# Kernel tuning notes

Measured on AMD Instinct MI355X. Metric: run time of the kernel, lower is better.

Reference implementation:

```python
import jax, jax.numpy as jnp
import numpy as np

IN_FEATURES = 1024
N_CLASSES = 50257
CUTOFFS = [2000, 10000]      # head covers [0,2000); clusters [2000,10000), [10000,50257)
DIV_VALUE = 4.0
IGNORE_INDEX = -1
N_ROWS = 4096
HEAD_SIZE = CUTOFFS[0] + len(CUTOFFS)  # 2002 (head classes + one slot per tail cluster)
HSZ = [int(IN_FEATURES // (DIV_VALUE ** (i + 1))) for i in range(len(CUTOFFS))]  # [256, 64]
BOUNDS = CUTOFFS + [N_CLASSES]


def setup_inputs() -> dict:
    key = jax.random.key(0)
    ks = jax.random.split(key, 8)
    x = jax.random.normal(ks[0], (N_ROWS, IN_FEATURES), dtype=jnp.float32)
    target = jax.random.randint(ks[1], (N_ROWS,), 0, N_CLASSES, dtype=jnp.int64)
    drop = jax.random.uniform(ks[2], (N_ROWS,)) < 0.1
    target = jnp.where(drop, IGNORE_INDEX, target)
    s = 1.0 / np.sqrt(IN_FEATURES)
    head_w = jax.random.normal(ks[3], (HEAD_SIZE, IN_FEATURES), dtype=jnp.float32) * s
    proj0 = jax.random.normal(ks[4], (HSZ[0], IN_FEATURES), dtype=jnp.float32) * s
    out0 = jax.random.normal(ks[5], (BOUNDS[1] - BOUNDS[0], HSZ[0]), dtype=jnp.float32) * (1.0 / np.sqrt(HSZ[0]))
    proj1 = jax.random.normal(ks[6], (HSZ[1], IN_FEATURES), dtype=jnp.float32) * s
    out1 = jax.random.normal(ks[7], (BOUNDS[2] - BOUNDS[1], HSZ[1]), dtype=jnp.float32) * (1.0 / np.sqrt(HSZ[1]))
    return {"x": x, "target": target, "head_w": head_w,
            "proj0": proj0, "out0": out0, "proj1": proj1, "out1": out1}


def reference(x, target, head_w, proj0, out0, proj1, out1):
    # head: [N, cutoff0 + n_clusters] logits, shared log-softmax
    head_lp = jax.nn.log_softmax(jnp.einsum('nd,hd->nh', x, head_w), axis=-1)
    rows = jnp.arange(x.shape[0])
    valid = target != IGNORE_INDEX
    t = jnp.where(valid, target, 0)

    # head-band targets: log prob directly from head
    t_head = jnp.clip(t, 0, CUTOFFS[0] - 1)
    logp = head_lp[rows, t_head]

    # tail clusters: head cluster-slot logprob + within-cluster logprob
    tails = [(proj0, out0), (proj1, out1)]
    for i, (proj, out) in enumerate(tails):
        low, high = BOUNDS[i], BOUNDS[i + 1]
        # [N, hsz] @ [hsz, osz] -> [N, osz] cluster logits
        cl_lp = jax.nn.log_softmax(
            jnp.einsum('nh,oh->no', jnp.einsum('nd,hd->nh', x, proj), out), axis=-1)
        rel = jnp.clip(t - low, 0, high - low - 1)
        cand = head_lp[:, CUTOFFS[0] + i] + cl_lp[rows, rel]
        logp = jnp.where((t >= low) & (t < high), cand, logp)

    # ignore-index filter + mean == masked mean over valid rows
    vf = valid.astype(logp.dtype)
    loss = -(logp * vf).sum() / vf.sum()
    return loss
```

## Files before the change

kernel.cpp:

```cpp
#include <hip/hip_runtime.h>
#include <hip/hip_bf16.h>

typedef __attribute__((ext_vector_type(8))) short bf16x8;
typedef __attribute__((ext_vector_type(4))) float f32x4;
typedef unsigned short u16;

constexpr int NR      = 4096;
constexpr int INF     = 1024;
constexpr int HEAD_N  = 2002;
constexpr int HEAD_NP = 2048;
constexpr int C0_LO   = 2000, C0_HI = 10000;
constexpr int C0_N    = 8000;
constexpr int C0_NP   = 8064;
constexpr int C1_N    = 40257;
constexpr int C1_NP   = 40320;
constexpr int K0      = 256;
constexpr int K1      = 64;
constexpr int PCAT    = 320;
constexpr int PCAT_P  = 384;
constexpr int WCAT_R  = HEAD_NP + PCAT_P;
constexpr int IGNORE  = -1;
constexpr float LOG2E = 1.4426950408889634f;
constexpr float LN2   = 0.6931471805599453f;

static __device__ __forceinline__ u16 f32_to_bf16(float f) {
    unsigned int u = __float_as_uint(f);
    return (u16)((u + 0x7FFFu + ((u >> 16) & 1u)) >> 16);
}

static __device__ __forceinline__ float fast_exp2(float x) {
#if __has_builtin(__builtin_amdgcn_exp2f)
    return __builtin_amdgcn_exp2f(x);
#else
    return __expf(x * LN2);
#endif
}

static __device__ __forceinline__ void gload_lds16(const u16* g, u16* l) {
    __builtin_amdgcn_global_load_lds(
        (const __attribute__((address_space(1))) unsigned int*)g,
        (__attribute__((address_space(3))) unsigned int*)l, 16, 0, 0);
}

struct CvtSegs { const float* s[6]; u16* d[6]; int n8[6]; float sc[6]; };

__global__ void cvt_multi(CvtSegs segs) {
    const int stride = gridDim.x * blockDim.x;
    const int gid = blockIdx.x * blockDim.x + threadIdx.x;
#pragma unroll
    for (int seg = 0; seg < 6; ++seg) {
        const float4* sp = (const float4*)segs.s[seg];
        bf16x8* dp = (bf16x8*)segs.d[seg];
        const int n8 = segs.n8[seg];
        const float sc = segs.sc[seg];
        for (int i = gid; i < n8; i += stride) {
            float4 a = sp[2 * i], b = sp[2 * i + 1];
            bf16x8 o;
            o[0] = (short)f32_to_bf16(a.x * sc); o[1] = (short)f32_to_bf16(a.y * sc);
            o[2] = (short)f32_to_bf16(a.z * sc); o[3] = (short)f32_to_bf16(a.w * sc);
            o[4] = (short)f32_to_bf16(b.x * sc); o[5] = (short)f32_to_bf16(b.y * sc);
            o[6] = (short)f32_to_bf16(b.z * sc); o[7] = (short)f32_to_bf16(b.w * sc);
            dp[i] = o;
        }
    }
}

__launch_bounds__(256, 2)
__global__ void fused_headproj(const u16* __restrict__ A, const u16* __restrict__ B,
                               const int* __restrict__ tgt,
                               float* __restrict__ SEH, float* __restrict__ TL,
                               float* __restrict__ HF, u16* __restrict__ HB)
{
    constexpr int K = INF;
    __shared__ u16 ldsA[128 * 64];
    __shared__ u16 ldsB[128 * 64];
    __shared__ int sth[128];
    const int tid  = threadIdx.x;
    const int wid  = tid >> 6;
    const int lane = tid & 63;
    const int wr   = wid >> 1;
    const int wc   = wid & 1;
    const int row0 = blockIdx.x * 128;
    const int col0 = blockIdx.y * 128;
    const bool expmode = (blockIdx.y < HEAD_NP / 128);

    if (expmode && tid < 128) {
        int t = tgt[row0 + tid];
        sth[tid] = (t < 0) ? 0 : (t < C0_LO ? t : (t < C0_HI ? C0_LO : C0_LO + 1));
    }

    f32x4 acc[4][4];
#pragma unroll
    for (int m = 0; m < 4; ++m)
#pragma unroll
        for (int n = 0; n < 4; ++n) acc[m][n] = (f32x4){0.f, 0.f, 0.f, 0.f};

    const int srow = lane >> 3;
    const int ssw  = (lane & 7) ^ srow;

    for (int ks = 0; ks < K / 64; ++ks) {
        const int k0 = ks * 64;
#pragma unroll
        for (int q = 0; q < 4; ++q) {
            const int c   = q * 4 + wid;
            const int row = c * 8 + srow;
            gload_lds16(A + (size_t)(row0 + row) * K + k0 + ssw * 8, ldsA + c * 512);
        }
#pragma unroll
        for (int q = 0; q < 4; ++q) {
            const int c   = q * 4 + wid;
            const int row = c * 8 + srow;
            gload_lds16(B + (size_t)(col0 + row) * K + k0 + ssw * 8, ldsB + c * 512);
        }
        __syncthreads();

        const bf16x8* A8 = (const bf16x8*)ldsA;
        const bf16x8* B8 = (const bf16x8*)ldsB;
        bf16x8 af[4][2], bf[4][2];
#pragma unroll
        for (int m = 0; m < 4; ++m) {
            const int ar = wr * 64 + m * 16 + (lane & 15);
#pragma unroll
            for (int ksub = 0; ksub < 2; ++ksub) {
                const int slot = ksub * 4 + (lane >> 4);
                af[m][ksub] = A8[ar * 8 + (slot ^ (ar & 7))];
            }
        }
#pragma unroll
        for (int n = 0; n < 4; ++n) {
            const int br = wc * 64 + n * 16 + (lane & 15);
#pragma unroll
            for (int ksub = 0; ksub < 2; ++ksub) {
                const int slot = ksub * 4 + (lane >> 4);
                bf[n][ksub] = B8[br * 8 + (slot ^ (br & 7))];
            }
        }
#pragma unroll
        for (int ksub = 0; ksub < 2; ++ksub)
#pragma unroll
            for (int m = 0; m < 4; ++m)
#pragma unroll
                for (int n = 0; n < 4; ++n)
                    acc[m][n] = __builtin_amdgcn_mfma_f32_16x16x32_bf16(
                        af[m][ksub], bf[n][ksub], acc[m][n], 0, 0, 0);
        __syncthreads();
    }

    if (expmode) {
#pragma unroll
        for (int m = 0; m < 4; ++m) {
            f32x4 rs = (f32x4){0.f, 0.f, 0.f, 0.f};
#pragma unroll
            for (int n = 0; n < 4; ++n) {
                const int cls = col0 + wc * 64 + n * 16 + (lane & 15);
                if (cls < HEAD_N) {
#pragma unroll
                    for (int r = 0; r < 4; ++r) {
                        rs[r] += fast_exp2(acc[m][n][r]);
                        const int lrow = wr * 64 + m * 16 + (lane >> 4) * 4 + r;
                        if (sth[lrow] == cls) TL[row0 + lrow] = acc[m][n][r];
                    }
                }
            }
#pragma unroll
            for (int msk = 1; msk < 16; msk <<= 1) {
#pragma unroll
                for (int r = 0; r < 4; ++r) rs[r] += __shfl_xor(rs[r], msk, 64);
            }
            if ((lane & 15) == 0) {
                const int rb = row0 + wr * 64 + m * 16 + (lane >> 4) * 4;
#pragma unroll
                for (int r = 0; r < 4; ++r) atomicAdd(&SEH[rb + r], rs[r]);
            }
        }
    } else {
        const int pc0 = col0 - HEAD_NP;
#pragma unroll
        for (int m = 0; m < 4; ++m) {
#pragma unroll
            for (int n = 0; n < 4; ++n) {
                const int col = pc0 + wc * 64 + n * 16 + (lane & 15);
                if (col < PCAT) {
#pragma unroll
                    for (int r = 0; r < 4; ++r) {
                        const int row = row0 + wr * 64 + m * 16 + (lane >> 4) * 4 + r;
                        const float v = acc[m][n][r];
                        HF[(size_t)row * PCAT + col] = v;
                        HB[(size_t)row * PCAT + col] = f32_to_bf16(v);
                    }
                }
            }
        }
    }
}

template<int K, int CT>
__launch_bounds__(256, 2)
__global__ void sumexp_stream(const u16* __restrict__ H, int ldh,
                              const u16* __restrict__ W,
                              int nreal, int tps, int ntiles,
                              float* __restrict__ SE)
{
    constexpr int MSETS = 2;
    constexpr int NKF   = K / 32;
    constexpr int SLOTS = K / 8;
    constexpr int NT    = CT / 16;
    constexpr int CHUNKS = CT * K * 2 / 4096;
    constexpr int RPC   = 256 / SLOTS;
    __shared__ u16 ldsB[2][CT * K];

    const int tid  = threadIdx.x;
    const int wid  = tid >> 6;
    const int lane = tid & 63;
    const int row0 = blockIdx.x * (4 * MSETS * 16) + wid * (MSETS * 16);

    const int t0 = blockIdx.y * tps;
    const int t1 = min(t0 + tps, ntiles);
    if (t0 >= t1) return;

    bf16x8 afr[MSETS][NKF];
#pragma unroll
    for (int m = 0; m < MSETS; ++m) {
        const u16* hr = H + (size_t)(row0 + m * 16 + (lane & 15)) * ldh + (lane >> 4) * 8;
#pragma unroll
        for (int kf = 0; kf < NKF; ++kf)
            afr[m][kf] = *(const bf16x8*)(hr + kf * 32);
    }

    float rs[MSETS][4];
#pragma unroll
    for (int m = 0; m < MSETS; ++m)
#pragma unroll
        for (int r = 0; r < 4; ++r) rs[m][r] = 0.f;

    const int trow   = tid / SLOTS;
    const int swoff  = ((tid % SLOTS) ^ (trow & 7)) * 8;

    auto STAGE = [&](int t, int buf) {
        const u16* wb = W + (size_t)t * CT * K + (size_t)trow * K + swoff;
        u16* lb = &ldsB[buf][wid * 512];
#pragma unroll
        for (int c = 0; c < CHUNKS; ++c)
            gload_lds16(wb + (size_t)c * RPC * K, lb + c * 2048);
    };

    int cur = 0;
    STAGE(t0, 0);
    __syncthreads();

    for (int t = t0; t < t1; ++t) {
        if (t + 1 < t1) STAGE(t + 1, cur ^ 1);

        const bf16x8* B8 = (const bf16x8*)ldsB[cur];
        const bool full = (t + 1) * CT <= nreal;
#pragma unroll
        for (int n = 0; n < NT; ++n) {
            const int br = n * 16 + (lane & 15);
            bf16x8 bfr[NKF];
#pragma unroll
            for (int kf = 0; kf < NKF; ++kf)
                bfr[kf] = B8[br * SLOTS + ((kf * 4 + (lane >> 4)) ^ (br & 7))];
            f32x4 acc[MSETS];
#pragma unroll
            for (int m = 0; m < MSETS; ++m) acc[m] = (f32x4){0.f, 0.f, 0.f, 0.f};
#pragma unroll
            for (int m = 0; m < MSETS; ++m)
#pragma unroll
                for (int kf = 0; kf < NKF; ++kf)
                    acc[m] = __builtin_amdgcn_mfma_f32_16x16x32_bf16(
                        afr[m][kf], bfr[kf], acc[m], 0, 0, 0);
            if (full) {
#pragma unroll
                for (int m = 0; m < MSETS; ++m)
#pragma unroll
                    for (int r = 0; r < 4; ++r) rs[m][r] += fast_exp2(acc[m][r]);
            } else {
                const int cls = t * CT + n * 16 + (lane & 15);
                if (cls < nreal) {
#pragma unroll
                    for (int m = 0; m < MSETS; ++m)
#pragma unroll
                        for (int r = 0; r < 4; ++r) rs[m][r] += fast_exp2(acc[m][r]);
                }
            }
        }
        __syncthreads();
        cur ^= 1;
    }

#pragma unroll
    for (int msk = 1; msk < 16; msk <<= 1)
#pragma unroll
        for (int m = 0; m < MSETS; ++m)
#pragma unroll
            for (int r = 0; r < 4; ++r)
                rs[m][r] += __shfl_xor(rs[m][r], msk, 64);
    if ((lane & 15) == 0) {
        const int rb = row0 + (lane >> 4) * 4;
#pragma unroll
        for (int m = 0; m < MSETS; ++m)
#pragma unroll
            for (int r = 0; r < 4; ++r)
                atomicAdd(&SE[rb + m * 16 + r], rs[m][r]);
    }
}

__global__ void epilogue_kernel(const int* __restrict__ tgt, const float* __restrict__ tl,
                                const float* __restrict__ out0, const float* __restrict__ out1,
                                const float* __restrict__ hcatf,
                                const float* __restrict__ se_head, const float* __restrict__ se_c0,
                                const float* __restrict__ se_c1,
                                float* __restrict__ rowlogp, float* __restrict__ rowvalid) {
    const int wid = threadIdx.x >> 6, lane = threadIdx.x & 63;
    const int r = blockIdx.x * 4 + wid;
    const int t = tgt[r];
    const bool valid = (t != IGNORE);
    const int tc = valid ? t : 0;
    const int band = (tc < C0_LO) ? 0 : (tc < C0_HI) ? 1 : 2;

    float p2 = 0.f;
    if (band == 1) {
        const float* hr = hcatf + (size_t)r * PCAT;
        const float* cr = out0 + (size_t)(tc - C0_LO) * K0;
        for (int k = lane; k < K0; k += 64) p2 += hr[k] * cr[k];
    } else if (band == 2) {
        p2 = hcatf[(size_t)r * PCAT + 256 + lane] * out1[(size_t)(tc - C0_HI) * K1 + lane];
    }
#pragma unroll
    for (int msk = 32; msk >= 1; msk >>= 1) p2 += __shfl_xor(p2, msk, 64);

    if (lane == 0) {
        float logp = LN2 * tl[r] - __logf(se_head[r]);
        if (band == 1)      logp += p2 - __logf(se_c0[r]);
        else if (band == 2) logp += p2 - __logf(se_c1[r]);
        rowlogp[r]  = valid ? logp : 0.f;
        rowvalid[r] = valid ? 1.f : 0.f;
    }
}

__global__ void final_reduce(const float* __restrict__ rowlogp,
                             const float* __restrict__ rowvalid, float* __restrict__ out) {
    __shared__ float sl[256], sv[256];
    const int tid = threadIdx.x;
    float a = 0.f, b = 0.f;
    for (int i = tid; i < NR; i += 256) { a += rowlogp[i]; b += rowvalid[i]; }
    sl[tid] = a; sv[tid] = b;
    __syncthreads();
    for (int s = 128; s > 0; s >>= 1) {
        if (tid < s) { sl[tid] += sl[tid + s]; sv[tid] += sv[tid + s]; }
        __syncthreads();
    }
    if (tid == 0) out[0] = -sl[0] / sv[0];
}

extern "C" void kernel_launch(void* const* d_in, const int* in_sizes, int n_in,
                              void* d_out, int out_size, void* d_ws, size_t ws_size,
                              hipStream_t stream) {
    const float* x      = (const float*)d_in[0];
    const int*   tgt    = (const int*)d_in[1];
    const float* head_w = (const float*)d_in[2];
    const float* proj0  = (const float*)d_in[3];
    const float* out0   = (const float*)d_in[4];
    const float* proj1  = (const float*)d_in[5];
    const float* out1   = (const float*)d_in[6];
    float* loss = (float*)d_out;

    char* base = (char*)d_ws;
    size_t off = 0;
    auto alloc = [&](size_t bytes) { char* p = base + off; off += (bytes + 255) & ~(size_t)255; return p; };

    u16* xb    = (u16*)alloc((size_t)NR * INF * 2);
    u16* wcatb = (u16*)alloc((size_t)WCAT_R * INF * 2);
    u16* o0b   = (u16*)alloc((size_t)C0_NP * K0 * 2);
    u16* o1b   = (u16*)alloc((size_t)C1_NP * K1 * 2);
    float* hcatf = (float*)alloc((size_t)NR * PCAT * 4);
    u16*   hcatb = (u16*)alloc((size_t)NR * PCAT * 2);
    float* se_head = (float*)alloc((size_t)NR * 4);
    float* se_c0   = (float*)alloc((size_t)NR * 4);
    float* se_c1   = (float*)alloc((size_t)NR * 4);
    float* tl       = (float*)alloc((size_t)NR * 4);
    float* rowlogp  = (float*)alloc((size_t)NR * 4);
    float* rowvalid = (float*)alloc((size_t)NR * 4);

    hipMemsetAsync(se_head, 0, (size_t)NR * 4, stream);
    hipMemsetAsync(se_c0,   0, (size_t)NR * 4, stream);
    hipMemsetAsync(se_c1,   0, (size_t)NR * 4, stream);

    CvtSegs segs;
    segs.s[0] = x;      segs.d[0] = xb;                              segs.n8[0] = NR * INF / 8;      segs.sc[0] = 1.0f;
    segs.s[1] = head_w; segs.d[1] = wcatb;                           segs.n8[1] = HEAD_N * INF / 8;  segs.sc[1] = LOG2E;
    segs.s[2] = proj0;  segs.d[2] = wcatb + (size_t)HEAD_NP * INF;   segs.n8[2] = 256 * INF / 8;     segs.sc[2] = 1.0f;
    segs.s[3] = proj1;  segs.d[3] = wcatb + (size_t)(HEAD_NP + 256) * INF; segs.n8[3] = 64 * INF / 8; segs.sc[3] = 1.0f;
    segs.s[4] = out0;   segs.d[4] = o0b;                             segs.n8[4] = C0_N * K0 / 8;     segs.sc[4] = LOG2E;
    segs.s[5] = out1;   segs.d[5] = o1b;                             segs.n8[5] = C1_N * K1 / 8;     segs.sc[5] = LOG2E;
    cvt_multi<<<2048, 256, 0, stream>>>(segs);

    fused_headproj<<<dim3(32, WCAT_R / 128), 256, 0, stream>>>(
        xb, wcatb, tgt, se_head, tl, hcatf, hcatb);

    sumexp_stream<K0, 32><<<dim3(32, 32), 256, 0, stream>>>(
        hcatb, PCAT, o0b, C0_N, 8, 250, se_c0);
    sumexp_stream<K1, 128><<<dim3(32, 40), 256, 0, stream>>>(
        hcatb + 256, PCAT, o1b, C1_N, 8, 315, se_c1);

    epilogue_kernel<<<NR / 4, 256, 0, stream>>>(tgt, tl, out0, out1, hcatf,
                                                se_head, se_c0, se_c1, rowlogp, rowvalid);
    final_reduce<<<1, 256, 0, stream>>>(rowlogp, rowvalid, loss);
    (void)in_sizes; (void)n_in; (void)out_size; (void)ws_size;
}
```

Baseline: 109.8 us.

## Compact tail-cluster rows by target and fuse head and cluster sumexp into one kernel

A new compaction kernel builds per-cluster row lists from the targets, so the cluster sum-exp GEMMs run only over rows whose target falls in that cluster instead of all 4096 rows. The head GEMM and both cluster sum-exp streams are merged into one interleaved mega-kernel launch, and the projection GEMM is split into its own small kernel. Atomics and memsets are replaced by per-split partial buffers that the epilogue reduces. This skips most of the cluster work, which is legitimate because the loss only needs the target row's cluster normaliser, at the cost of gather loads and an extra serial launch.

```diff
diff --git a/kernel.cpp b/kernel.cpp
--- a/kernel.cpp
+++ b/kernel.cpp
@@ -11,7 +11,6 @@
 constexpr int HEAD_NP = 2048;
 constexpr int C0_LO   = 2000, C0_HI = 10000;
 constexpr int C0_N    = 8000;
-constexpr int C0_NP   = 8064;
 constexpr int C1_N    = 40257;
 constexpr int C1_NP   = 40320;
 constexpr int K0      = 256;
@@ -22,6 +21,11 @@
 constexpr int IGNORE  = -1;
 constexpr float LOG2E = 1.4426950408889634f;
 constexpr float LN2   = 0.6931471805599453f;
+
+constexpr int S0      = 16;
+constexpr int S1      = 10;
+constexpr int NHP     = 32;
+constexpr int MEGA_GRID = 1024 + 512;
 
 static __device__ __forceinline__ u16 f32_to_bf16(float f) {
     unsigned int u = __float_as_uint(f);
@@ -65,26 +69,117 @@
     }
 }
 
+__global__ void compact_kernel(const int* __restrict__ tgt,
+                               int* __restrict__ c0list, int* __restrict__ c1list,
+                               int* __restrict__ crow, int* __restrict__ cnts) {
+    __shared__ int b0, b1;
+    if (threadIdx.x == 0) { b0 = 0; b1 = 0; }
+    __syncthreads();
+#pragma unroll
+    for (int i = 0; i < 4; ++i) {
+        const int r = threadIdx.x + i * 1024;
+        const int t = tgt[r];
+        if (t >= C0_LO && t < C0_HI) { int s = atomicAdd(&b0, 1); c0list[s] = r; crow[r] = s; }
+        else if (t >= C0_HI)         { int s = atomicAdd(&b1, 1); c1list[s] = r; crow[r] = s; }
+        else crow[r] = 0;
+    }
+    __syncthreads();
+    const int c0 = b0, c1 = b1;
+    const int p0 = (c0 + 127) & ~127, p1 = (c1 + 127) & ~127;
+    if (threadIdx.x == 0) { cnts[0] = c0; cnts[1] = c1; cnts[2] = p0; cnts[3] = p1; }
+    for (int i = c0 + (int)threadIdx.x; i < p0; i += 1024) c0list[i] = 0;
+    for (int i = c1 + (int)threadIdx.x; i < p1; i += 1024) c1list[i] = 0;
+}
+
 __launch_bounds__(256, 2)
-__global__ void fused_headproj(const u16* __restrict__ A, const u16* __restrict__ B,
-                               const int* __restrict__ tgt,
-                               float* __restrict__ SEH, float* __restrict__ TL,
-                               float* __restrict__ HF, u16* __restrict__ HB)
+__global__ void proj_tile(const u16* __restrict__ A, const u16* __restrict__ B,
+                          float* __restrict__ HF, u16* __restrict__ HB)
 {
     constexpr int K = INF;
     __shared__ u16 ldsA[128 * 64];
     __shared__ u16 ldsB[128 * 64];
-    __shared__ int sth[128];
-    const int tid  = threadIdx.x;
-    const int wid  = tid >> 6;
-    const int lane = tid & 63;
-    const int wr   = wid >> 1;
-    const int wc   = wid & 1;
-    const int row0 = blockIdx.x * 128;
-    const int col0 = blockIdx.y * 128;
-    const bool expmode = (blockIdx.y < HEAD_NP / 128);
-
-    if (expmode && tid < 128) {
+    const int tid = threadIdx.x, wid = tid >> 6, lane = tid & 63;
+    const int wr = wid >> 1, wc = wid & 1;
+    const int row0 = blockIdx.x * 128, col0 = blockIdx.y * 128;
+
+    f32x4 acc[4][4];
+#pragma unroll
+    for (int m = 0; m < 4; ++m)
+#pragma unroll
+        for (int n = 0; n < 4; ++n) acc[m][n] = (f32x4){0.f, 0.f, 0.f, 0.f};
+
+    const int srow = lane >> 3;
+    const int ssw  = (lane & 7) ^ srow;
+
+    for (int ks = 0; ks < K / 64; ++ks) {
+        const int k0 = ks * 64;
+#pragma unroll
+        for (int q = 0; q < 4; ++q) {
+            const int c = q * 4 + wid, row = c * 8 + srow;
+            gload_lds16(A + (size_t)(row0 + row) * K + k0 + ssw * 8, ldsA + c * 512);
+        }
+#pragma unroll
+        for (int q = 0; q < 4; ++q) {
+            const int c = q * 4 + wid, row = c * 8 + srow;
+            gload_lds16(B + (size_t)(col0 + row) * K + k0 + ssw * 8, ldsB + c * 512);
+        }
+        __syncthreads();
+        const bf16x8* A8 = (const bf16x8*)ldsA;
+        const bf16x8* B8 = (const bf16x8*)ldsB;
+        bf16x8 af[4][2], bfr[4][2];
+#pragma unroll
+        for (int m = 0; m < 4; ++m) {
+            const int ar = wr * 64 + m * 16 + (lane & 15);
+#pragma unroll
+            for (int ks2 = 0; ks2 < 2; ++ks2)
+                af[m][ks2] = A8[ar * 8 + ((ks2 * 4 + (lane >> 4)) ^ (ar & 7))];
+        }
+#pragma unroll
+        for (int n = 0; n < 4; ++n) {
+            const int br = wc * 64 + n * 16 + (lane & 15);
+#pragma unroll
+            for (int ks2 = 0; ks2 < 2; ++ks2)
+                bfr[n][ks2] = B8[br * 8 + ((ks2 * 4 + (lane >> 4)) ^ (br & 7))];
+        }
+#pragma unroll
+        for (int ks2 = 0; ks2 < 2; ++ks2)
+#pragma unroll
+            for (int m = 0; m < 4; ++m)
+#pragma unroll
+                for (int n = 0; n < 4; ++n)
+                    acc[m][n] = __builtin_amdgcn_mfma_f32_16x16x32_bf16(
+                        af[m][ks2], bfr[n][ks2], acc[m][n], 0, 0, 0);
+        __syncthreads();
+    }
+#pragma unroll
+    for (int m = 0; m < 4; ++m)
+#pragma unroll
+        for (int n = 0; n < 4; ++n) {
+            const int col = col0 + wc * 64 + n * 16 + (lane & 15);
+            if (col < PCAT) {
+#pragma unroll
+                for (int r = 0; r < 4; ++r) {
+                    const int row = row0 + wr * 64 + m * 16 + (lane >> 4) * 4 + r;
+                    const float v = acc[m][n][r];
+                    HF[(size_t)row * PCAT + col] = v;
+                    HB[(size_t)row * PCAT + col] = f32_to_bf16(v);
+                }
+            }
+        }
+}
+
+static __device__ void head_section(int rb, int ct,
+                                    const u16* __restrict__ A, const u16* __restrict__ B,
+                                    const int* __restrict__ tgt,
+                                    float* __restrict__ SEHp, float* __restrict__ TL,
+                                    u16* ldsA, u16* ldsB, int* sth)
+{
+    constexpr int K = INF;
+    const int tid = threadIdx.x, wid = tid >> 6, lane = tid & 63;
+    const int wr = wid >> 1, wc = wid & 1;
+    const int row0 = rb * 128, col0 = ct * 128;
+
+    if (tid < 128) {
         int t = tgt[row0 + tid];
         sth[tid] = (t < 0) ? 0 : (t < C0_LO ? t : (t < C0_HI ? C0_LO : C0_LO + 1));
     }
@@ -102,126 +197,97 @@
         const int k0 = ks * 64;
 #pragma unroll
         for (int q = 0; q < 4; ++q) {
-            const int c   = q * 4 + wid;
-            const int row = c * 8 + srow;
+            const int c = q * 4 + wid, row = c * 8 + srow;
             gload_lds16(A + (size_t)(row0 + row) * K + k0 + ssw * 8, ldsA + c * 512);
         }
 #pragma unroll
         for (int q = 0; q < 4; ++q) {
-            const int c   = q * 4 + wid;
-            const int row = c * 8 + srow;
+            const int c = q * 4 + wid, row = c * 8 + srow;
             gload_lds16(B + (size_t)(col0 + row) * K + k0 + ssw * 8, ldsB + c * 512);
         }
         __syncthreads();
-
         const bf16x8* A8 = (const bf16x8*)ldsA;
         const bf16x8* B8 = (const bf16x8*)ldsB;
-        bf16x8 af[4][2], bf[4][2];
+        bf16x8 af[4][2], bfr[4][2];
 #pragma unroll
         for (int m = 0; m < 4; ++m) {
             const int ar = wr * 64 + m * 16 + (lane & 15);
 #pragma unroll
-            for (int ksub = 0; ksub < 2; ++ksub) {
-                const int slot = ksub * 4 + (lane >> 4);
-                af[m][ksub] = A8[ar * 8 + (slot ^ (ar & 7))];
-            }
+            for (int ks2 = 0; ks2 < 2; ++ks2)
+                af[m][ks2] = A8[ar * 8 + ((ks2 * 4 + (lane >> 4)) ^ (ar & 7))];
         }
 #pragma unroll
         for (int n = 0; n < 4; ++n) {
             const int br = wc * 64 + n * 16 + (lane & 15);
 #pragma unroll
-            for (int ksub = 0; ksub < 2; ++ksub) {
-                const int slot = ksub * 4 + (lane >> 4);
-                bf[n][ksub] = B8[br * 8 + (slot ^ (br & 7))];
-            }
-        }
-#pragma unroll
-        for (int ksub = 0; ksub < 2; ++ksub)
+            for (int ks2 = 0; ks2 < 2; ++ks2)
+                bfr[n][ks2] = B8[br * 8 + ((ks2 * 4 + (lane >> 4)) ^ (br & 7))];
+        }
+#pragma unroll
+        for (int ks2 = 0; ks2 < 2; ++ks2)
 #pragma unroll
             for (int m = 0; m < 4; ++m)
 #pragma unroll
                 for (int n = 0; n < 4; ++n)
                     acc[m][n] = __builtin_amdgcn_mfma_f32_16x16x32_bf16(
-                        af[m][ksub], bf[n][ksub], acc[m][n], 0, 0, 0);
+                        af[m][ks2], bfr[n][ks2], acc[m][n], 0, 0, 0);
         __syncthreads();
     }
 
-    if (expmode) {
-#pragma unroll
-        for (int m = 0; m < 4; ++m) {
-            f32x4 rs = (f32x4){0.f, 0.f, 0.f, 0.f};
-#pragma unroll
-            for (int n = 0; n < 4; ++n) {
-                const int cls = col0 + wc * 64 + n * 16 + (lane & 15);
-                if (cls < HEAD_N) {
-#pragma unroll
-                    for (int r = 0; r < 4; ++r) {
-                        rs[r] += fast_exp2(acc[m][n][r]);
-                        const int lrow = wr * 64 + m * 16 + (lane >> 4) * 4 + r;
-                        if (sth[lrow] == cls) TL[row0 + lrow] = acc[m][n][r];
-                    }
+    const int slot = ct * 2 + wc;
+#pragma unroll
+    for (int m = 0; m < 4; ++m) {
+        f32x4 rs = (f32x4){0.f, 0.f, 0.f, 0.f};
+#pragma unroll
+        for (int n = 0; n < 4; ++n) {
+            const int cls = col0 + wc * 64 + n * 16 + (lane & 15);
+            if (cls < HEAD_N) {
+#pragma unroll
+                for (int r = 0; r < 4; ++r) {
+                    rs[r] += fast_exp2(acc[m][n][r]);
+                    const int lrow = wr * 64 + m * 16 + (lane >> 4) * 4 + r;
+                    if (sth[lrow] == cls) TL[row0 + lrow] = acc[m][n][r];
                 }
             }
-#pragma unroll
-            for (int msk = 1; msk < 16; msk <<= 1) {
-#pragma unroll
-                for (int r = 0; r < 4; ++r) rs[r] += __shfl_xor(rs[r], msk, 64);
-            }
-            if ((lane & 15) == 0) {
-                const int rb = row0 + wr * 64 + m * 16 + (lane >> 4) * 4;
-#pragma unroll
-                for (int r = 0; r < 4; ++r) atomicAdd(&SEH[rb + r], rs[r]);
-            }
-        }
-    } else {
-        const int pc0 = col0 - HEAD_NP;
-#pragma unroll
-        for (int m = 0; m < 4; ++m) {
-#pragma unroll
-            for (int n = 0; n < 4; ++n) {
-                const int col = pc0 + wc * 64 + n * 16 + (lane & 15);
-                if (col < PCAT) {
-#pragma unroll
-                    for (int r = 0; r < 4; ++r) {
-                        const int row = row0 + wr * 64 + m * 16 + (lane >> 4) * 4 + r;
-                        const float v = acc[m][n][r];
-                        HF[(size_t)row * PCAT + col] = v;
-                        HB[(size_t)row * PCAT + col] = f32_to_bf16(v);
-                    }
-                }
-            }
+        }
+#pragma unroll
+        for (int msk = 1; msk < 16; msk <<= 1)
+#pragma unroll
+            for (int r = 0; r < 4; ++r) rs[r] += __shfl_xor(rs[r], msk, 64);
+        if ((lane & 15) == 0) {
+            const int rbase = row0 + wr * 64 + m * 16 + (lane >> 4) * 4;
+#pragma unroll
+            for (int r = 0; r < 4; ++r) SEHp[(size_t)slot * NR + rbase + r] = rs[r];
         }
     }
 }
 
 template<int K, int CT>
-__launch_bounds__(256, 2)
-__global__ void sumexp_stream(const u16* __restrict__ H, int ldh,
-                              const u16* __restrict__ W,
-                              int nreal, int tps, int ntiles,
-                              float* __restrict__ SE)
+static __device__ void sumexp_section(const u16* __restrict__ Hbase, int ldh,
+                                      const int* __restrict__ list,
+                                      const u16* __restrict__ W,
+                                      int nreal, int ntiles, int tps,
+                                      int rb, int split, float* __restrict__ SEp,
+                                      u16* lds)
 {
     constexpr int MSETS = 2;
     constexpr int NKF   = K / 32;
     constexpr int SLOTS = K / 8;
-    constexpr int NT    = CT / 16;
     constexpr int CHUNKS = CT * K * 2 / 4096;
     constexpr int RPC   = 256 / SLOTS;
-    __shared__ u16 ldsB[2][CT * K];
-
-    const int tid  = threadIdx.x;
-    const int wid  = tid >> 6;
-    const int lane = tid & 63;
-    const int row0 = blockIdx.x * (4 * MSETS * 16) + wid * (MSETS * 16);
-
-    const int t0 = blockIdx.y * tps;
+    constexpr int NT    = CT / 16;
+
+    const int tid = threadIdx.x, wid = tid >> 6, lane = tid & 63;
+    const int row0 = rb * 128 + wid * 32;
+
+    const int t0 = split * tps;
     const int t1 = min(t0 + tps, ntiles);
-    if (t0 >= t1) return;
 
     bf16x8 afr[MSETS][NKF];
 #pragma unroll
     for (int m = 0; m < MSETS; ++m) {
-        const u16* hr = H + (size_t)(row0 + m * 16 + (lane & 15)) * ldh + (lane >> 4) * 8;
+        const int orow = list[row0 + m * 16 + (lane & 15)];
+        const u16* hr = Hbase + (size_t)orow * ldh + (lane >> 4) * 8;
 #pragma unroll
         for (int kf = 0; kf < NKF; ++kf)
             afr[m][kf] = *(const bf16x8*)(hr + kf * 32);
@@ -233,12 +299,12 @@
 #pragma unroll
         for (int r = 0; r < 4; ++r) rs[m][r] = 0.f;
 
-    const int trow   = tid / SLOTS;
-    const int swoff  = ((tid % SLOTS) ^ (trow & 7)) * 8;
+    const int trow  = tid / SLOTS;
+    const int swoff = ((tid % SLOTS) ^ (trow & 7)) * 8;
 
     auto STAGE = [&](int t, int buf) {
         const u16* wb = W + (size_t)t * CT * K + (size_t)trow * K + swoff;
-        u16* lb = &ldsB[buf][wid * 512];
+        u16* lb = lds + buf * (CT * K) + wid * 512;
 #pragma unroll
         for (int c = 0; c < CHUNKS; ++c)
             gload_lds16(wb + (size_t)c * RPC * K, lb + c * 2048);
@@ -250,8 +316,7 @@
 
     for (int t = t0; t < t1; ++t) {
         if (t + 1 < t1) STAGE(t + 1, cur ^ 1);
-
-        const bf16x8* B8 = (const bf16x8*)ldsB[cur];
+        const bf16x8* B8 = (const bf16x8*)(lds + cur * (CT * K));
         const bool full = (t + 1) * CT <= nreal;
 #pragma unroll
         for (int n = 0; n < NT; ++n) {
@@ -269,19 +334,11 @@
                 for (int kf = 0; kf < NKF; ++kf)
                     acc[m] = __builtin_amdgcn_mfma_f32_16x16x32_bf16(
                         afr[m][kf], bfr[kf], acc[m], 0, 0, 0);
-            if (full) {
+            if (full || (t * CT + n * 16 + (lane & 15)) < nreal) {
 #pragma unroll
                 for (int m = 0; m < MSETS; ++m)
 #pragma unroll
                     for (int r = 0; r < 4; ++r) rs[m][r] += fast_exp2(acc[m][r]);
-            } else {
-                const int cls = t * CT + n * 16 + (lane & 15);
-                if (cls < nreal) {
-#pragma unroll
-                    for (int m = 0; m < MSETS; ++m)
-#pragma unroll
-                        for (int r = 0; r < 4; ++r) rs[m][r] += fast_exp2(acc[m][r]);
-                }
             }
         }
         __syncthreads();
@@ -293,23 +350,57 @@
 #pragma unroll
         for (int m = 0; m < MSETS; ++m)
 #pragma unroll
+            for (int r = 0; r < 4; ++r) rs[m][r] += __shfl_xor(rs[m][r], msk, 64);
+    if ((lane & 15) == 0) {
+        const int rbase = row0 + (lane >> 4) * 4;
+#pragma unroll
+        for (int m = 0; m < MSETS; ++m)
+#pragma unroll
             for (int r = 0; r < 4; ++r)
-                rs[m][r] += __shfl_xor(rs[m][r], msk, 64);
-    if ((lane & 15) == 0) {
-        const int rb = row0 + (lane >> 4) * 4;
-#pragma unroll
-        for (int m = 0; m < MSETS; ++m)
-#pragma unroll
-            for (int r = 0; r < 4; ++r)
-                atomicAdd(&SE[rb + m * 16 + r], rs[m][r]);
+                SEp[(size_t)split * NR + rbase + m * 16 + r] = rs[m][r];
+    }
+}
+
+__launch_bounds__(256, 3)
+__global__ void mega_kernel(const u16* __restrict__ xb, const u16* __restrict__ wcatb,
+                            const u16* __restrict__ hcatb,
+                            const u16* __restrict__ o0b, const u16* __restrict__ o1b,
+                            const int* __restrict__ tgt,
+                            const int* __restrict__ c0list, const int* __restrict__ c1list,
+                            const int* __restrict__ cnts,
+                            float* __restrict__ SEHp, float* __restrict__ TL,
+                            float* __restrict__ C0p, float* __restrict__ C1p)
+{
+    __shared__ u16 smem[2][8192];
+    __shared__ int sth[128];
+    const int bid = blockIdx.x;
+
+    if (bid < 1024) {
+        if ((bid & 1) == 0) {
+            const int h = bid >> 1;
+            head_section(h >> 4, h & 15, xb, wcatb, tgt, SEHp, TL,
+                         smem[0], smem[1], sth);
+        } else {
+            const int c = bid >> 1;
+            const int rb = c / S1, split = c - rb * S1;
+            if (rb * 128 < cnts[3])
+                sumexp_section<K1, 128>(hcatb + 256, PCAT, c1list, o1b,
+                                        C1_N, C1_NP / 128, 32, rb, split, C1p, smem[0]);
+        }
+    } else {
+        const int idx = bid - 1024;
+        const int rb = idx >> 4, split = idx & 15;
+        if (rb * 128 < cnts[2])
+            sumexp_section<K0, 32>(hcatb, PCAT, c0list, o0b,
+                                   C0_N, C0_N / 32, 16, rb, split, C0p, smem[0]);
     }
 }
 
 __global__ void epilogue_kernel(const int* __restrict__ tgt, const float* __restrict__ tl,
                                 const float* __restrict__ out0, const float* __restrict__ out1,
                                 const float* __restrict__ hcatf,
-                                const float* __restrict__ se_head, const float* __restrict__ se_c0,
-                                const float* __restrict__ se_c1,
+                                const float* __restrict__ SEHp, const float* __restrict__ C0p,
+                                const float* __restrict__ C1p, const int* __restrict__ crow,
                                 float* __restrict__ rowlogp, float* __restrict__ rowvalid) {
     const int wid = threadIdx.x >> 6, lane = threadIdx.x & 63;
     const int r = blockIdx.x * 4 + wid;
@@ -317,22 +408,32 @@
     const bool valid = (t != IGNORE);
     const int tc = valid ? t : 0;
     const int band = (tc < C0_LO) ? 0 : (tc < C0_HI) ? 1 : 2;
+    const int cr = crow[r];
 
     float p2 = 0.f;
     if (band == 1) {
         const float* hr = hcatf + (size_t)r * PCAT;
-        const float* cr = out0 + (size_t)(tc - C0_LO) * K0;
-        for (int k = lane; k < K0; k += 64) p2 += hr[k] * cr[k];
+        const float* crp = out0 + (size_t)(tc - C0_LO) * K0;
+        for (int k = lane; k < K0; k += 64) p2 += hr[k] * crp[k];
     } else if (band == 2) {
         p2 = hcatf[(size_t)r * PCAT + 256 + lane] * out1[(size_t)(tc - C0_HI) * K1 + lane];
     }
 #pragma unroll
     for (int msk = 32; msk >= 1; msk >>= 1) p2 += __shfl_xor(p2, msk, 64);
 
+    float hp = (lane < NHP) ? SEHp[(size_t)lane * NR + r] : 0.f;
+    float cp = 0.f;
+    if (band == 1 && lane < S0) cp = C0p[(size_t)lane * NR + cr];
+    if (band == 2 && lane < S1) cp = C1p[(size_t)lane * NR + cr];
+#pragma unroll
+    for (int msk = 1; msk < 32; msk <<= 1) {
+        hp += __shfl_xor(hp, msk, 64);
+        cp += __shfl_xor(cp, msk, 64);
+    }
+
     if (lane == 0) {
-        float logp = LN2 * tl[r] - __logf(se_head[r]);
-        if (band == 1)      logp += p2 - __logf(se_c0[r]);
-        else if (band == 2) logp += p2 - __logf(se_c1[r]);
+        float logp = LN2 * tl[r] - __logf(hp);
+        if (band != 0) logp += p2 - __logf(cp);
         rowlogp[r]  = valid ? logp : 0.f;
         rowvalid[r] = valid ? 1.f : 0.f;
     }
@@ -371,20 +472,22 @@
 
     u16* xb    = (u16*)alloc((size_t)NR * INF * 2);
     u16* wcatb = (u16*)alloc((size_t)WCAT_R * INF * 2);
-    u16* o0b   = (u16*)alloc((size_t)C0_NP * K0 * 2);
+    u16* o0b   = (u16*)alloc((size_t)C0_N * K0 * 2);
     u16* o1b   = (u16*)alloc((size_t)C1_NP * K1 * 2);
     float* hcatf = (float*)alloc((size_t)NR * PCAT * 4);
     u16*   hcatb = (u16*)alloc((size_t)NR * PCAT * 2);
-    float* se_head = (float*)alloc((size_t)NR * 4);
-    float* se_c0   = (float*)alloc((size_t)NR * 4);
-    float* se_c1   = (float*)alloc((size_t)NR * 4);
-    float* tl       = (float*)alloc((size_t)NR * 4);
+    float* SEHp = (float*)alloc((size_t)NHP * NR * 4);
+    float* C0p  = (float*)alloc((size_t)S0 * NR * 4);
+    float* C1p  = (float*)alloc((size_t)S1 * NR * 4);
+    float* tl   = (float*)alloc((size_t)NR * 4);
+    int* c0list = (int*)alloc((size_t)(NR + 128) * 4);
+    int* c1list = (int*)alloc((size_t)(NR + 128) * 4);
+    int* crow   = (int*)alloc((size_t)NR * 4);
+    int* cnts   = (int*)alloc(4 * 4);
     float* rowlogp  = (float*)alloc((size_t)NR * 4);
     float* rowvalid = (float*)alloc((size_t)NR * 4);
 
-    hipMemsetAsync(se_head, 0, (size_t)NR * 4, stream);
-    hipMemsetAsync(se_c0,   0, (size_t)NR * 4, stream);
-    hipMemsetAsync(se_c1,   0, (size_t)NR * 4, stream);
+    compact_kernel<<<1, 1024, 0, stream>>>(tgt, c0list, c1list, crow, cnts);
 
     CvtSegs segs;
     segs.s[0] = x;      segs.d[0] = xb;                              segs.n8[0] = NR * INF / 8;      segs.sc[0] = 1.0f;
@@ -395,16 +498,13 @@
     segs.s[5] = out1;   segs.d[5] = o1b;                             segs.n8[5] = C1_N * K1 / 8;     segs.sc[5] = LOG2E;
     cvt_multi<<<2048, 256, 0, stream>>>(segs);
 
-    fused_headproj<<<dim3(32, WCAT_R / 128), 256, 0, stream>>>(
-        xb, wcatb, tgt, se_head, tl, hcatf, hcatb);
-
-    sumexp_stream<K0, 32><<<dim3(32, 32), 256, 0, stream>>>(
-        hcatb, PCAT, o0b, C0_N, 8, 250, se_c0);
-    sumexp_stream<K1, 128><<<dim3(32, 40), 256, 0, stream>>>(
-        hcatb + 256, PCAT, o1b, C1_N, 8, 315, se_c1);
+    proj_tile<<<dim3(32, PCAT_P / 128), 256, 0, stream>>>(xb, wcatb + (size_t)HEAD_NP * INF, hcatf, hcatb);
+
+    mega_kernel<<<MEGA_GRID, 256, 0, stream>>>(xb, wcatb, hcatb, o0b, o1b, tgt,
+                                               c0list, c1list, cnts, SEHp, tl, C0p, C1p);
 
     epilogue_kernel<<<NR / 4, 256, 0, stream>>>(tgt, tl, out0, out1, hcatf,
-                                                se_head, se_c0, se_c1, rowlogp, rowvalid);
+                                                SEHp, C0p, C1p, crow, rowlogp, rowvalid);
     final_reduce<<<1, 256, 0, stream>>>(rowlogp, rowvalid, loss);
     (void)in_sizes; (void)n_in; (void)out_size; (void)ws_size;
 }
```

After: 100.5 us. -8.5%, faster.
